# Performance work log

Hardware: AMD Instinct MI355X
Metric: run time of the kernel (lower is better)

The kernel has to match this reference:

```python
import jax, jax.numpy as jnp
import numpy as np

B, S, D = 2, 1024, 128


def setup_inputs() -> dict:
    key = jax.random.key(0)
    k1, k2, k3 = jax.random.split(key, 3)
    node_features = jax.random.normal(k1, (B, S, D), dtype=jnp.float32)
    # Linear(2D -> D) then Linear(D -> 1); weights stored as (in, out)
    W1 = jax.random.normal(k2, (2 * D, D), dtype=jnp.float32) * (1.0 / np.sqrt(2 * D))
    b1 = jnp.zeros((D,), dtype=jnp.float32)
    W2 = jax.random.normal(k3, (D, 1), dtype=jnp.float32) * (1.0 / np.sqrt(D))
    b2 = jnp.zeros((1,), dtype=jnp.float32)
    return {"node_features": node_features, "W1": W1, "b1": b1, "W2": W2, "b2": b2}


def reference(node_features, W1, b1, W2, b2):
    # Faithful to: concat(node_i, node_j) @ W1 + b1 -> relu -> @ W2 + b2.
    # Since concat([xi, xj]) @ W1 == xi @ W1[:D] + xj @ W1[D:], project nodes
    # once (O(S*D^2)) and broadcast-add per pair instead of materializing the
    # (B,S,S,2D) concatenated tensor.
    d = node_features.shape[-1]
    hi = node_features @ W1[:d]   # (B,S,D) contribution of node_i
    hj = node_features @ W1[d:]   # (B,S,D) contribution of node_j
    h = jax.nn.relu(hi[:, :, None, :] + hj[:, None, :, :] + b1)  # (B,S,S,D)
    edge_logits = jnp.einsum('bijd,d->bij', h, W2[:, 0]) + b2[0]  # (B,S,S)
    return edge_logits
```

## Files before the change

### kernel.cpp

```cpp
#include <hip/hip_runtime.h>

#define BB 2
#define SDIM 1024
#define DDIM 128
#define K1_ROWS 4

#define F4GET(v,k) ((k)==0?(v).x:((k)==1?(v).y:((k)==2?(v).z:(v).w)))

typedef _Float16 h2v __attribute__((ext_vector_type(2)));
typedef _Float16 h8v __attribute__((ext_vector_type(8)));

__device__ __forceinline__ h2v habs2(h2v t) {
    unsigned u = __builtin_bit_cast(unsigned, t) & 0x7FFF7FFFu;
    return __builtin_bit_cast(h2v, u);
}

__device__ __forceinline__ float hdot2(h2v a, h2v b, float acc) {
#if __has_builtin(__builtin_amdgcn_fdot2)
    return __builtin_amdgcn_fdot2(a, b, acc, false);
#else
    acc = fmaf((float)a.x, (float)b.x, acc);
    return fmaf((float)a.y, (float)b.y, acc);
#endif
}

__global__ __launch_bounds__(256) void proj_kernel(
    const float* __restrict__ x, const float* __restrict__ W1,
    const float* __restrict__ b1, const float* __restrict__ W2,
    const float* __restrict__ b2,
    ushort* __restrict__ hi16, ushort* __restrict__ hjb16,
    float* __restrict__ si2, float* __restrict__ sj2)
{
    __shared__ float sX[K1_ROWS][DDIM];
    __shared__ float sRed[4][K1_ROWS];
    const int tid  = threadIdx.x;
    const int d    = tid & 127;
    const int half = tid >> 7;
    const int r0   = blockIdx.x * K1_ROWS;

    if (tid < K1_ROWS * DDIM / 4) {
        reinterpret_cast<float4*>(&sX[0][0])[tid] =
            reinterpret_cast<const float4*>(x + (size_t)r0 * DDIM)[tid];
    }
    __syncthreads();

    const float* Wh = W1 + (size_t)half * DDIM * DDIM;

    float acc[K1_ROWS];
    #pragma unroll
    for (int r = 0; r < K1_ROWS; ++r) acc[r] = 0.f;

    #pragma unroll 4
    for (int k = 0; k < DDIM; k += 4) {
        float4 xv[K1_ROWS];
        #pragma unroll
        for (int r = 0; r < K1_ROWS; ++r)
            xv[r] = *reinterpret_cast<const float4*>(&sX[r][k]);
        #pragma unroll
        for (int kk = 0; kk < 4; ++kk) {
            float w = Wh[(size_t)(k + kk) * DDIM + d];
            #pragma unroll
            for (int r = 0; r < K1_ROWS; ++r)
                acc[r] = fmaf(F4GET(xv[r], kk), w, acc[r]);
        }
    }

    if (half) {
        const float bv = b1[d];
        #pragma unroll
        for (int r = 0; r < K1_ROWS; ++r) acc[r] += bv;
    }

    ushort* hout = half ? hjb16 : hi16;
    #pragma unroll
    for (int r = 0; r < K1_ROWS; ++r) {
        _Float16 hv = (_Float16)acc[r];
        hout[(size_t)(r0 + r) * DDIM + d] = __builtin_bit_cast(ushort, hv);
    }

    const float wv = W2[d];
    const int lane = tid & 63;
    const int wave = tid >> 6;
    #pragma unroll
    for (int r = 0; r < K1_ROWS; ++r) {
        float v = acc[r] * wv;
        #pragma unroll
        for (int off = 32; off >= 1; off >>= 1)
            v += __shfl_xor(v, off, 64);
        if (lane == 0) sRed[wave][r] = v;
    }
    __syncthreads();
    if (tid < K1_ROWS) {
        si2[r0 + tid] = 0.5f * (sRed[0][tid] + sRed[1][tid]);
    } else if (tid < 2 * K1_ROWS) {
        int r = tid - K1_ROWS;
        sj2[r0 + r] = 0.5f * (sRed[2][r] + sRed[3][r]) + b2[0];
    }
}

__global__ __launch_bounds__(256) void edge_kernel(
    const ushort* __restrict__ hi16, const ushort* __restrict__ hjb16,
    const float* __restrict__ si2, const float* __restrict__ sj2,
    const float* __restrict__ W2, float* __restrict__ out)
{
    __shared__ ushort sHi[64 * DDIM];
    __shared__ ushort sHj[64 * DDIM];
    __shared__ ushort sWh[DDIM];
    __shared__ float  sSi[64];
    __shared__ float  sSj[64];

    const int b   = blockIdx.z;
    const int i0  = blockIdx.y * 64;
    const int j0  = blockIdx.x * 64;
    const int tid = threadIdx.x;

    {
        const h8v* srcI = reinterpret_cast<const h8v*>(hi16  + ((size_t)b * SDIM + i0) * DDIM);
        const h8v* srcJ = reinterpret_cast<const h8v*>(hjb16 + ((size_t)b * SDIM + j0) * DDIM);
        h8v* dI = reinterpret_cast<h8v*>(sHi);
        h8v* dJ = reinterpret_cast<h8v*>(sHj);
        #pragma unroll
        for (int p = 0; p < 4; ++p) {
            int idx = p * 256 + tid;
            int row = idx >> 4, ch = idx & 15;
            dI[row * 16 + (ch ^ (row & 7))]        = srcI[idx];
            dJ[row * 16 + (ch ^ ((row >> 2) & 7))] = srcJ[idx];
        }
    }
    if (tid < DDIM) {
        _Float16 wv = (_Float16)(0.5f * W2[tid]);
        sWh[tid] = __builtin_bit_cast(ushort, wv);
    } else if (tid < DDIM + 64) {
        sSi[tid - DDIM] = si2[b * SDIM + i0 + (tid - DDIM)];
    } else {
        sSj[tid - DDIM - 64] = sj2[b * SDIM + j0 + (tid - DDIM - 64)];
    }
    __syncthreads();

    const int tx = tid & 15;
    const int ty = tid >> 4;
    const int ri = ty * 4;
    const int cj = tx * 4;
    const int bswz = tx & 7;

    float acc[4][4];
    #pragma unroll
    for (int r = 0; r < 4; ++r)
        #pragma unroll
        for (int c = 0; c < 4; ++c) acc[r][c] = 0.f;

    const h8v* sAi = reinterpret_cast<const h8v*>(sHi);
    const h8v* sBj = reinterpret_cast<const h8v*>(sHj);
    const h8v* sWv = reinterpret_cast<const h8v*>(sWh);

    #pragma unroll 2
    for (int ch = 0; ch < 16; ++ch) {
        h8v A[4], Bv[4];
        #pragma unroll
        for (int r = 0; r < 4; ++r)
            A[r] = sAi[(ri + r) * 16 + (ch ^ ((ri + r) & 7))];
        #pragma unroll
        for (int c = 0; c < 4; ++c)
            Bv[c] = sBj[(cj + c) * 16 + (ch ^ bswz)];
        const h8v Wv = sWv[ch];

        #pragma unroll
        for (int r = 0; r < 4; ++r) {
            const h2v* ap = reinterpret_cast<const h2v*>(&A[r]);
            #pragma unroll
            for (int c = 0; c < 4; ++c) {
                const h2v* bp = reinterpret_cast<const h2v*>(&Bv[c]);
                const h2v* wp = reinterpret_cast<const h2v*>(&Wv);
                float a = acc[r][c];
                #pragma unroll
                for (int k = 0; k < 4; ++k) {
                    h2v t = ap[k] + bp[k];
                    a = hdot2(habs2(t), wp[k], a);
                }
                acc[r][c] = a;
            }
        }
    }

    #pragma unroll
    for (int r = 0; r < 4; ++r) {
        const float sv = sSi[ri + r];
        float4 o;
        o.x = acc[r][0] + sv + sSj[cj + 0];
        o.y = acc[r][1] + sv + sSj[cj + 1];
        o.z = acc[r][2] + sv + sSj[cj + 2];
        o.w = acc[r][3] + sv + sSj[cj + 3];
        size_t base = (size_t)b * SDIM * SDIM + (size_t)(i0 + ri + r) * SDIM + j0 + cj;
        *reinterpret_cast<float4*>(out + base) = o;
    }
}

extern "C" void kernel_launch(void* const* d_in, const int* in_sizes, int n_in,
                              void* d_out, int out_size, void* d_ws, size_t ws_size,
                              hipStream_t stream) {
    const float* x  = (const float*)d_in[0];
    const float* W1 = (const float*)d_in[1];
    const float* b1 = (const float*)d_in[2];
    const float* W2 = (const float*)d_in[3];
    const float* b2 = (const float*)d_in[4];
    float* out = (float*)d_out;

    char* ws = (char*)d_ws;
    ushort* hi16  = (ushort*)ws;
    ushort* hjb16 = hi16 + (size_t)BB * SDIM * DDIM;
    float*  si2   = (float*)(hjb16 + (size_t)BB * SDIM * DDIM);
    float*  sj2   = si2 + (size_t)BB * SDIM;

    proj_kernel<<<BB * SDIM / K1_ROWS, 256, 0, stream>>>(x, W1, b1, W2, b2, hi16, hjb16, si2, sj2);
    edge_kernel<<<dim3(SDIM / 64, SDIM / 64, BB), 256, 0, stream>>>(hi16, hjb16, si2, sj2, W2, out);
}
```

Measured before the change: 28.13 us.

## Use packed fp16 FMA accumulators in edge kernel and split-K projection

The edge kernel now accumulates |hi+hj|*w with packed half-precision FMA into two fp16 accumulator pairs instead of fdot2 into fp32. That roughly halves the per-element instruction cost, at the cost of accuracy from fp16 accumulation. The projection kernel is restructured to process 8 rows per block with a split-K across two thread halves, with the i/j halves moved to grid.y. The LDS swizzle is also changed to one unified row-XOR pattern shared by A and B tiles.

```diff
diff --git a/kernel.cpp b/kernel.cpp
--- a/kernel.cpp
+++ b/kernel.cpp
@@ -3,7 +3,6 @@
 #define BB 2
 #define SDIM 1024
 #define DDIM 128
-#define K1_ROWS 4
 
 #define F4GET(v,k) ((k)==0?(v).x:((k)==1?(v).y:((k)==2?(v).z:(v).w)))
 
@@ -15,13 +14,16 @@
     return __builtin_bit_cast(h2v, u);
 }
 
-__device__ __forceinline__ float hdot2(h2v a, h2v b, float acc) {
-#if __has_builtin(__builtin_amdgcn_fdot2)
-    return __builtin_amdgcn_fdot2(a, b, acc, false);
+__device__ __forceinline__ h2v hfma2(h2v a, h2v b, h2v c) {
+#if __has_builtin(__builtin_elementwise_fma)
+    return __builtin_elementwise_fma(a, b, c);
 #else
-    acc = fmaf((float)a.x, (float)b.x, acc);
-    return fmaf((float)a.y, (float)b.y, acc);
+    return a * b + c;
 #endif
+}
+
+__device__ __forceinline__ int rswz(int row) {
+    return (row & 7) ^ ((row >> 3) & 7);
 }
 
 __global__ __launch_bounds__(256) void proj_kernel(
@@ -31,70 +33,68 @@
     ushort* __restrict__ hi16, ushort* __restrict__ hjb16,
     float* __restrict__ si2, float* __restrict__ sj2)
 {
-    __shared__ float sX[K1_ROWS][DDIM];
-    __shared__ float sRed[4][K1_ROWS];
+    __shared__ float sX[8][DDIM];
+    __shared__ float sH[8][DDIM];
+    __shared__ float sRed[2][8];
     const int tid  = threadIdx.x;
     const int d    = tid & 127;
-    const int half = tid >> 7;
-    const int r0   = blockIdx.x * K1_ROWS;
-
-    if (tid < K1_ROWS * DDIM / 4) {
-        reinterpret_cast<float4*>(&sX[0][0])[tid] =
-            reinterpret_cast<const float4*>(x + (size_t)r0 * DDIM)[tid];
-    }
-    __syncthreads();
-
-    const float* Wh = W1 + (size_t)half * DDIM * DDIM;
-
-    float acc[K1_ROWS];
-    #pragma unroll
-    for (int r = 0; r < K1_ROWS; ++r) acc[r] = 0.f;
+    const int kh   = tid >> 7;
+    const int half = blockIdx.y;
+    const int r0   = blockIdx.x * 8;
+
+    reinterpret_cast<float4*>(&sX[0][0])[tid] =
+        reinterpret_cast<const float4*>(x + (size_t)r0 * DDIM)[tid];
+    __syncthreads();
+
+    const float* Wp = W1 + ((size_t)half * DDIM + kh * 64) * DDIM + d;
+
+    float acc[8];
+    #pragma unroll
+    for (int r = 0; r < 8; ++r) acc[r] = 0.f;
 
     #pragma unroll 4
-    for (int k = 0; k < DDIM; k += 4) {
-        float4 xv[K1_ROWS];
-        #pragma unroll
-        for (int r = 0; r < K1_ROWS; ++r)
-            xv[r] = *reinterpret_cast<const float4*>(&sX[r][k]);
+    for (int kc = 0; kc < 16; ++kc) {
+        float4 xv[8];
+        #pragma unroll
+        for (int r = 0; r < 8; ++r)
+            xv[r] = *reinterpret_cast<const float4*>(&sX[r][kh * 64 + kc * 4]);
         #pragma unroll
         for (int kk = 0; kk < 4; ++kk) {
-            float w = Wh[(size_t)(k + kk) * DDIM + d];
+            const float w = Wp[(size_t)(kc * 4 + kk) * DDIM];
             #pragma unroll
-            for (int r = 0; r < K1_ROWS; ++r)
+            for (int r = 0; r < 8; ++r)
                 acc[r] = fmaf(F4GET(xv[r], kk), w, acc[r]);
         }
     }
 
-    if (half) {
-        const float bv = b1[d];
-        #pragma unroll
-        for (int r = 0; r < K1_ROWS; ++r) acc[r] += bv;
-    }
-
-    ushort* hout = half ? hjb16 : hi16;
-    #pragma unroll
-    for (int r = 0; r < K1_ROWS; ++r) {
-        _Float16 hv = (_Float16)acc[r];
-        hout[(size_t)(r0 + r) * DDIM + d] = __builtin_bit_cast(ushort, hv);
-    }
-
-    const float wv = W2[d];
-    const int lane = tid & 63;
-    const int wave = tid >> 6;
-    #pragma unroll
-    for (int r = 0; r < K1_ROWS; ++r) {
-        float v = acc[r] * wv;
-        #pragma unroll
-        for (int off = 32; off >= 1; off >>= 1)
-            v += __shfl_xor(v, off, 64);
-        if (lane == 0) sRed[wave][r] = v;
-    }
-    __syncthreads();
-    if (tid < K1_ROWS) {
-        si2[r0 + tid] = 0.5f * (sRed[0][tid] + sRed[1][tid]);
-    } else if (tid < 2 * K1_ROWS) {
-        int r = tid - K1_ROWS;
-        sj2[r0 + r] = 0.5f * (sRed[2][r] + sRed[3][r]) + b2[0];
+    if (kh == 1) {
+        #pragma unroll
+        for (int r = 0; r < 8; ++r) sH[r][d] = acc[r];
+    }
+    __syncthreads();
+    if (kh == 0) {
+        const float bv = half ? b1[d] : 0.f;
+        const float wv = W2[d];
+        ushort* hout = half ? hjb16 : hi16;
+        const int lane = tid & 63;
+        const int wave = tid >> 6;
+        #pragma unroll
+        for (int r = 0; r < 8; ++r) {
+            float h = acc[r] + sH[r][d] + bv;
+            _Float16 hv = (_Float16)h;
+            hout[(size_t)(r0 + r) * DDIM + d] = __builtin_bit_cast(ushort, hv);
+            float v = h * wv;
+            #pragma unroll
+            for (int off = 32; off >= 1; off >>= 1)
+                v += __shfl_xor(v, off, 64);
+            if (lane == 0) sRed[wave][r] = v;
+        }
+    }
+    __syncthreads();
+    if (tid < 8) {
+        float s = 0.5f * (sRed[0][tid] + sRed[1][tid]);
+        if (half == 0) si2[r0 + tid] = s;
+        else           sj2[r0 + tid] = s + b2[0];
     }
 }
 
@@ -123,8 +123,9 @@
         for (int p = 0; p < 4; ++p) {
             int idx = p * 256 + tid;
             int row = idx >> 4, ch = idx & 15;
-            dI[row * 16 + (ch ^ (row & 7))]        = srcI[idx];
-            dJ[row * 16 + (ch ^ ((row >> 2) & 7))] = srcJ[idx];
+            int cs  = ch ^ rswz(row);
+            dI[row * 16 + cs] = srcI[idx];
+            dJ[row * 16 + cs] = srcJ[idx];
         }
     }
     if (tid < DDIM) {
@@ -141,13 +142,21 @@
     const int ty = tid >> 4;
     const int ri = ty * 4;
     const int cj = tx * 4;
-    const int bswz = tx & 7;
-
-    float acc[4][4];
+
+    int swzA[4], swzB[4];
+    #pragma unroll
+    for (int r = 0; r < 4; ++r) swzA[r] = rswz(ri + r);
+    #pragma unroll
+    for (int c = 0; c < 4; ++c) swzB[c] = rswz(cj + c);
+
+    h2v accP[4][4], accQ[4][4];
     #pragma unroll
     for (int r = 0; r < 4; ++r)
         #pragma unroll
-        for (int c = 0; c < 4; ++c) acc[r][c] = 0.f;
+        for (int c = 0; c < 4; ++c) {
+            accP[r][c] = (h2v)(_Float16)0;
+            accQ[r][c] = (h2v)(_Float16)0;
+        }
 
     const h8v* sAi = reinterpret_cast<const h8v*>(sHi);
     const h8v* sBj = reinterpret_cast<const h8v*>(sHj);
@@ -158,11 +167,12 @@
         h8v A[4], Bv[4];
         #pragma unroll
         for (int r = 0; r < 4; ++r)
-            A[r] = sAi[(ri + r) * 16 + (ch ^ ((ri + r) & 7))];
+            A[r] = sAi[(ri + r) * 16 + (ch ^ swzA[r])];
         #pragma unroll
         for (int c = 0; c < 4; ++c)
-            Bv[c] = sBj[(cj + c) * 16 + (ch ^ bswz)];
+            Bv[c] = sBj[(cj + c) * 16 + (ch ^ swzB[c])];
         const h8v Wv = sWv[ch];
+        const h2v* wp = reinterpret_cast<const h2v*>(&Wv);
 
         #pragma unroll
         for (int r = 0; r < 4; ++r) {
@@ -170,14 +180,14 @@
             #pragma unroll
             for (int c = 0; c < 4; ++c) {
                 const h2v* bp = reinterpret_cast<const h2v*>(&Bv[c]);
-                const h2v* wp = reinterpret_cast<const h2v*>(&Wv);
-                float a = acc[r][c];
-                #pragma unroll
-                for (int k = 0; k < 4; ++k) {
-                    h2v t = ap[k] + bp[k];
-                    a = hdot2(habs2(t), wp[k], a);
-                }
-                acc[r][c] = a;
+                h2v t0 = ap[0] + bp[0];
+                h2v t1 = ap[1] + bp[1];
+                h2v t2 = ap[2] + bp[2];
+                h2v t3 = ap[3] + bp[3];
+                accP[r][c] = hfma2(habs2(t0), wp[0], accP[r][c]);
+                accP[r][c] = hfma2(habs2(t1), wp[1], accP[r][c]);
+                accQ[r][c] = hfma2(habs2(t2), wp[2], accQ[r][c]);
+                accQ[r][c] = hfma2(habs2(t3), wp[3], accQ[r][c]);
             }
         }
     }
@@ -186,10 +196,14 @@
     for (int r = 0; r < 4; ++r) {
         const float sv = sSi[ri + r];
         float4 o;
-        o.x = acc[r][0] + sv + sSj[cj + 0];
-        o.y = acc[r][1] + sv + sSj[cj + 1];
-        o.z = acc[r][2] + sv + sSj[cj + 2];
-        o.w = acc[r][3] + sv + sSj[cj + 3];
+        o.x = ((float)accP[r][0].x + (float)accP[r][0].y)
+            + ((float)accQ[r][0].x + (float)accQ[r][0].y) + sv + sSj[cj + 0];
+        o.y = ((float)accP[r][1].x + (float)accP[r][1].y)
+            + ((float)accQ[r][1].x + (float)accQ[r][1].y) + sv + sSj[cj + 1];
+        o.z = ((float)accP[r][2].x + (float)accP[r][2].y)
+            + ((float)accQ[r][2].x + (float)accQ[r][2].y) + sv + sSj[cj + 2];
+        o.w = ((float)accP[r][3].x + (float)accP[r][3].y)
+            + ((float)accQ[r][3].x + (float)accQ[r][3].y) + sv + sSj[cj + 3];
         size_t base = (size_t)b * SDIM * SDIM + (size_t)(i0 + ri + r) * SDIM + j0 + cj;
         *reinterpret_cast<float4*>(out + base) = o;
     }
@@ -211,6 +225,6 @@
     float*  si2   = (float*)(hjb16 + (size_t)BB * SDIM * DDIM);
     float*  sj2   = si2 + (size_t)BB * SDIM;
 
-    proj_kernel<<<BB * SDIM / K1_ROWS, 256, 0, stream>>>(x, W1, b1, W2, b2, hi16, hjb16, si2, sj2);
+    proj_kernel<<<dim3(BB * SDIM / 8, 2), 256, 0, stream>>>(x, W1, b1, W2, b2, hi16, hjb16, si2, sj2);
     edge_kernel<<<dim3(SDIM / 64, SDIM / 64, BB), 256, 0, stream>>>(hi16, hjb16, si2, sj2, W2, out);
 }
```

After: 28.93 us. +2.8%, slower.
